# Performance work log

Hardware: AMD Instinct MI355X
Metric: run time of the kernel (lower is better)

The kernel has to match this reference:

```python
import jax, jax.numpy as jnp
import numpy as np

PATCH, STRIDE, TOPK, EPS = 16, 8, 8, 1e-8

def _leaky(x):
    return jax.nn.leaky_relu(x, 0.01)

def setup_inputs() -> dict:
    key = jax.random.key(0)
    ks = jax.random.split(key, 12)
    s = 0.05  # small weight scale to avoid tanh saturation
    return {
        "X":      jax.random.normal(ks[0], (16, 4096, 512), jnp.float32),
        "W_enc1": jax.random.normal(ks[1], (512, 256), jnp.float32) * s,
        "b_enc1": jax.random.normal(ks[2], (256,), jnp.float32) * s,
        "W_enc2": jax.random.normal(ks[3], (256, 64), jnp.float32) * s,
        "b_enc2": jax.random.normal(ks[4], (64,), jnp.float32) * s,
        "Wq":     jax.random.normal(ks[5], (64, 64), jnp.float32) * s,
        "Wk":     jax.random.normal(ks[6], (64, 64), jnp.float32) * s,
        "Wv":     jax.random.normal(ks[7], (64, 64), jnp.float32) * s,
        "W_agg":  jax.random.normal(ks[8], (64, 64), jnp.float32) * s,
        "b_agg":  jax.random.normal(ks[9], (64,), jnp.float32) * s,
        "W_dec":  jax.random.normal(ks[10], (64, 512), jnp.float32) * s,
        "b_dec":  jax.random.normal(ks[11], (512,), jnp.float32) * s,
    }

def reference(X, W_enc1, b_enc1, W_enc2, b_enc2, Wq, Wk, Wv, W_agg, b_agg, W_dec, b_dec):
    B, L, D = X.shape
    # var_encoder (dropout-free MLP)
    Xe = _leaky(X @ W_enc1 + b_enc1) @ W_enc2 + b_enc2          # (B, L, d)
    d = Xe.shape[-1]
    # unfold into overlapping patches
    h = (L - PATCH) // STRIDE + 1
    pos = jnp.arange(h)[:, None] * STRIDE + jnp.arange(PATCH)[None, :]  # (h, PATCH)
    patches = Xe[:, pos, :]                                      # (B, h, PATCH, d)
    per_patch = patches.mean(axis=2).reshape(B * h, d)           # (N, d)
    q = per_patch @ Wq
    k = per_patch @ Wk
    v = per_patch @ Wv                                           # (N, hqk)
    qn = q / (jnp.linalg.norm(q, axis=-1, keepdims=True) + EPS)
    kn = k / (jnp.linalg.norm(k, axis=-1, keepdims=True) + EPS)
    # antisymmetric outer product, (N, hqk, hqk)
    M = qn[:, :, None] * kn[:, None, :] - kn[:, :, None] * qn[:, None, :]
    A = jax.nn.relu(jnp.tanh(M))
    n = A.shape[-1]
    # topk pruning along last dim via scatter-style mask
    _, idx = jax.lax.top_k(A, TOPK)                              # (N, n, TOPK)
    mask = jnp.any(idx[..., None] == jnp.arange(n), axis=-2)     # (N, n, n) bool
    A = A * mask.astype(A.dtype)
    A = A / jnp.maximum(A.sum(axis=-1, keepdims=True), EPS)
    Av = jnp.einsum('nij,nj->ni', A, v)                          # (N, hqk)
    # after_agg (dropout = identity in eval)
    z = _leaky(Av @ W_agg + b_agg)                               # (N, d)
    zB = z.reshape(B, h, d)
    # overlap-add fold: each patch writes its (constant-over-time) z to its window
    seg = jnp.broadcast_to(zB[:, :, None, :], (B, h, PATCH, d)).reshape(B, h * PATCH, d)
    flat_pos = pos.reshape(-1)                                   # (h*PATCH,)
    out = jnp.zeros((B, L, d), X.dtype).at[:, flat_pos, :].add(seg)
    counts = jnp.zeros((L,), X.dtype).at[flat_pos].add(1.0)
    out = out / jnp.maximum(counts, 1.0)[None, :, None]
    return out @ W_dec + b_dec                                   # (B, L, D)
```

## Files before the change

### kernel.cpp

```cpp
#include <hip/hip_runtime.h>


typedef __attribute__((ext_vector_type(8))) _Float16 half8;
typedef __attribute__((ext_vector_type(4))) _Float16 half4;
typedef __attribute__((ext_vector_type(4))) float floatx4;

__device__ __forceinline__ _Float16 f2h(float f) { return (_Float16)f; }

#define MFMA16(A, B, C) __builtin_amdgcn_mfma_f32_16x16x32_f16((A), (B), (C), 0, 0, 0)

__global__ __launch_bounds__(256) void prep_weights(
    const float* __restrict__ W1, const float* __restrict__ W2,
    const float* __restrict__ Wd,
    _Float16* __restrict__ W1t, _Float16* __restrict__ W2t,
    _Float16* __restrict__ Wdt)
{
    int idx = blockIdx.x * 256 + threadIdx.x;
    { int n = idx >> 9, k = idx & 511;  W1t[idx] = f2h(W1[k * 256 + n]); }
    if (idx < 16384) { int n = idx >> 8, k = idx & 255; W2t[idx] = f2h(W2[k * 64 + n]); }
    if (idx < 32768) { int n = idx >> 6, k = idx & 63;  Wdt[idx] = f2h(Wd[k * 512 + n]); }
}

__global__ __launch_bounds__(256) void enc_fused(
    const float* __restrict__ X, const _Float16* __restrict__ W1t,
    const float* __restrict__ b1, const _Float16* __restrict__ W2t,
    const float* __restrict__ b2, float* __restrict__ Gs)
{
    __shared__ _Float16 smem[20992];
    _Float16* As   = smem;
    _Float16* Bs   = smem + 4608;
    _Float16* Hs16 = smem;

    const int tid  = threadIdx.x;
    const int lane = tid & 63;
    const int w    = tid >> 6;
    const int m0   = blockIdx.x * 64;

    const int arow  = tid >> 2;
    const int akseg = (tid & 3) << 4;
    const float* Abase = X + (size_t)(m0 + arow) * 512 + akseg;

    const int brow0  = (w << 6) + (lane >> 3);
    const int bchunk = (((lane & 7) ^ ((lane >> 3) & 7)) << 3);

    floatx4 acc1[4][4];
#pragma unroll
    for (int ci = 0; ci < 4; ci++)
#pragma unroll
        for (int mi = 0; mi < 4; mi++) acc1[ci][mi] = (floatx4){0.f, 0.f, 0.f, 0.f};

    float4 pa[4];
    auto loadA = [&](int kt) {
#pragma unroll
        for (int u = 0; u < 4; u++) pa[u] = *(const float4*)(Abase + kt + 4 * u);
    };

    loadA(0);
    for (int kt = 0; kt < 512; kt += 64) {
#pragma unroll
        for (int inst = 0; inst < 8; inst++) {
            const _Float16* src = W1t + (size_t)(brow0 + inst * 8) * 512 + kt + bchunk;
            __builtin_amdgcn_global_load_lds(
                (const __attribute__((address_space(1))) unsigned int*)src,
                (__attribute__((address_space(3))) unsigned int*)(Bs + ((w << 6) + inst * 8) * 64),
                16, 0, 0);
        }
        {
            _Float16* d = &As[arow * 72 + akseg];
#pragma unroll
            for (int h = 0; h < 2; h++) {
                float4 f0 = pa[2 * h], f1 = pa[2 * h + 1];
                half8 o;
                o[0] = f2h(f0.x); o[1] = f2h(f0.y); o[2] = f2h(f0.z); o[3] = f2h(f0.w);
                o[4] = f2h(f1.x); o[5] = f2h(f1.y); o[6] = f2h(f1.z); o[7] = f2h(f1.w);
                *(half8*)(d + 8 * h) = o;
            }
        }
        __syncthreads();
        if (kt + 64 < 512) loadA(kt + 64);
#pragma unroll
        for (int ks = 0; ks < 2; ks++) {
            const int lchunk = ks * 4 + (lane >> 4);
            half8 af[4], bf[4];
#pragma unroll
            for (int ci = 0; ci < 4; ci++) {
                const int c = (w << 6) + ci * 16 + (lane & 15);
                af[ci] = *(const half8*)&Bs[c * 64 + ((lchunk ^ (lane & 7)) << 3)];
            }
#pragma unroll
            for (int mi = 0; mi < 4; mi++)
                bf[mi] = *(const half8*)&As[(mi * 16 + (lane & 15)) * 72 + ks * 32 + ((lane >> 4) << 3)];
#pragma unroll
            for (int ci = 0; ci < 4; ci++)
#pragma unroll
                for (int mi = 0; mi < 4; mi++)
                    acc1[ci][mi] = MFMA16(af[ci], bf[mi], acc1[ci][mi]);
        }
        __syncthreads();
    }

    float4 b1v[4];
#pragma unroll
    for (int ci = 0; ci < 4; ci++)
        b1v[ci] = *(const float4*)&b1[(w << 6) + ci * 16 + ((lane >> 4) << 2)];
#pragma unroll
    for (int ci = 0; ci < 4; ci++) {
#pragma unroll
        for (int mi = 0; mi < 4; mi++) {
            float vs[4];
#pragma unroll
            for (int r = 0; r < 4; r++) {
                float v = acc1[ci][mi][r] + ((const float*)&b1v[ci])[r];
                vs[r] = v > 0.f ? v : 0.01f * v;
            }
#pragma unroll
            for (int r = 0; r < 4; r++) {
                vs[r] += __shfl_xor(vs[r], 1);
                vs[r] += __shfl_xor(vs[r], 2);
                vs[r] += __shfl_xor(vs[r], 4);
            }
            if ((lane & 7) == 0) {
                const int gl = 2 * mi + ((lane & 15) >> 3);
                half4 hv;
#pragma unroll
                for (int r = 0; r < 4; r++) hv[r] = f2h(vs[r]);
                *(half4*)&Hs16[gl * 264 + (w << 6) + ci * 16 + ((lane >> 4) << 2)] = hv;
            }
        }
    }
    __syncthreads();

    floatx4 acc2 = (floatx4){0.f, 0.f, 0.f, 0.f};
    const int kq = (lane >> 4) << 3;
#pragma unroll
    for (int ks = 0; ks < 8; ks++) {
        half8 af = *(const half8*)&Hs16[(lane & 15) * 264 + ks * 32 + kq];
        half8 bf = *(const half8*)&W2t[(size_t)((w << 4) + (lane & 15)) * 256 + ks * 32 + kq];
        acc2 = MFMA16(af, bf, acc2);
    }
    if (lane < 32) {
        const int n = (w << 4) + (lane & 15);
        const float bb = 8.f * b2[n];
        const int gbase = blockIdx.x * 8;
#pragma unroll
        for (int r = 0; r < 4; r++) {
            const int g = ((lane >> 4) << 2) + r;
            Gs[(size_t)(gbase + g) * 64 + n] = acc2[r] + bb;
        }
    }
}

#define TOP8_INS(mv) do { float _x = (mv); float _t;            \
    _t = fmaxf(s0,_x); _x = fminf(s0,_x); s0 = _t;              \
    _t = fmaxf(s1,_x); _x = fminf(s1,_x); s1 = _t;              \
    _t = fmaxf(s2,_x); _x = fminf(s2,_x); s2 = _t;              \
    _t = fmaxf(s3,_x); _x = fminf(s3,_x); s3 = _t;              \
    _t = fmaxf(s4,_x); _x = fminf(s4,_x); s4 = _t;              \
    _t = fmaxf(s5,_x); _x = fminf(s5,_x); s5 = _t;              \
    _t = fmaxf(s6,_x); _x = fminf(s6,_x); s6 = _t;              \
    s7 = fmaxf(s7,_x); } while (0)

__global__ __launch_bounds__(256) void patch_attn(
    const float* __restrict__ Gs,  const float* __restrict__ Wq,
    const float* __restrict__ Wk,  const float* __restrict__ Wv,
    const float* __restrict__ Wagg, const float* __restrict__ bagg,
    float* __restrict__ zout)
{
    __shared__ float sh[4][336];
    const int w    = threadIdx.x >> 6;
    const int lane = threadIdx.x & 63;
    const int n = blockIdx.x * 4 + w;
    const int b = n / 511;
    const int i = n - b * 511;
    float* pp  = &sh[w][0];
    float* qs  = pp + 64;
    float* ksm = pp + 128;
    float* vsm = pp + 192;
    float* avs = pp + 256;

    const float* gp = Gs + ((size_t)(b * 512 + i)) * 64 + lane;
    pp[lane] = (gp[0] + gp[64]) * 0.0625f;
    __syncthreads();

    float q = 0.f, k = 0.f, v = 0.f;
#pragma unroll 4
    for (int e = 0; e < 64; e += 4) {
        float4 p4 = *(const float4*)&pp[e];
        q = fmaf(p4.x, Wq[(e+0)*64+lane], q); q = fmaf(p4.y, Wq[(e+1)*64+lane], q);
        q = fmaf(p4.z, Wq[(e+2)*64+lane], q); q = fmaf(p4.w, Wq[(e+3)*64+lane], q);
        k = fmaf(p4.x, Wk[(e+0)*64+lane], k); k = fmaf(p4.y, Wk[(e+1)*64+lane], k);
        k = fmaf(p4.z, Wk[(e+2)*64+lane], k); k = fmaf(p4.w, Wk[(e+3)*64+lane], k);
        v = fmaf(p4.x, Wv[(e+0)*64+lane], v); v = fmaf(p4.y, Wv[(e+1)*64+lane], v);
        v = fmaf(p4.z, Wv[(e+2)*64+lane], v); v = fmaf(p4.w, Wv[(e+3)*64+lane], v);
    }
    float sq = q * q, sk = k * k;
#pragma unroll
    for (int o = 1; o < 64; o <<= 1) { sq += __shfl_xor(sq, o); sk += __shfl_xor(sk, o); }
    const float qni = q / (sqrtf(sq) + 1e-8f);
    const float kni = k / (sqrtf(sk) + 1e-8f);
    qs[lane] = qni; ksm[lane] = kni; vsm[lane] = v;
    __syncthreads();

    auto MV = [&](float kj, float qj) { return fmaf(qni, kj, -(kni * qj)); };

    float s0=-1e30f,s1=-1e30f,s2=-1e30f,s3=-1e30f,s4=-1e30f,s5=-1e30f,s6=-1e30f,s7=-1e30f;
#pragma unroll
    for (int j = 0; j < 64; j += 4) {
        float4 k4 = *(const float4*)&ksm[j];
        float4 q4 = *(const float4*)&qs[j];
        TOP8_INS(MV(k4.x, q4.x)); TOP8_INS(MV(k4.y, q4.y));
        TOP8_INS(MV(k4.z, q4.z)); TOP8_INS(MV(k4.w, q4.w));
    }
    const float teff = fmaxf(s7, 1e-37f) * (1.f - 1.2e-7f);

    float ssum = 0.f, av = 0.f;
#pragma unroll
    for (int j = 0; j < 64; j += 4) {
        float4 k4 = *(const float4*)&ksm[j];
        float4 q4 = *(const float4*)&qs[j];
        float4 v4 = *(const float4*)&vsm[j];
#define P2(KJ, QJ, VJ) do { float _m = MV(KJ, QJ); float _x2 = _m * _m;           \
        float _a = _m * (15.f + _x2) * __builtin_amdgcn_rcpf(fmaf(6.f, _x2, 15.f)); \
        float _am = (_m >= teff) ? _a : 0.f;                                       \
        ssum += _am; av = fmaf(_am, (VJ), av); } while (0)
        P2(k4.x, q4.x, v4.x); P2(k4.y, q4.y, v4.y);
        P2(k4.z, q4.z, v4.z); P2(k4.w, q4.w, v4.w);
#undef P2
    }
    avs[lane] = av / fmaxf(ssum, 1e-8f);
    __syncthreads();

    float zc = bagg[lane];
#pragma unroll 4
    for (int e = 0; e < 64; e += 4) {
        float4 a4 = *(const float4*)&avs[e];
        zc = fmaf(a4.x, Wagg[(e+0)*64+lane], zc); zc = fmaf(a4.y, Wagg[(e+1)*64+lane], zc);
        zc = fmaf(a4.z, Wagg[(e+2)*64+lane], zc); zc = fmaf(a4.w, Wagg[(e+3)*64+lane], zc);
    }
    zc = zc > 0.f ? zc : 0.01f * zc;
    zout[(size_t)n * 64 + lane] = zc;
}

__global__ __launch_bounds__(256) void dec_fused(
    const float* __restrict__ z, const _Float16* __restrict__ Wdt,
    const float* __restrict__ bd, float* __restrict__ out)
{
    __shared__ _Float16 As[128 * 72];
    __shared__ _Float16 Bs[128 * 72];
    const int tid  = threadIdx.x;
    const int lane = tid & 63;
    const int w    = tid >> 6;
    const int m0 = blockIdx.y * 128, n0 = blockIdx.x * 128;
    const int wrow = (w & 1) << 6, wcol = (w >> 1) << 6;

    {
        const int arow  = tid >> 1;
        const int akseg = (tid & 1) << 5;
        const int row = m0 + arow;
        const int b = row >> 12, l = row & 4095, g = l >> 3;
        const int g0 = g - 1 >= 0 ? g - 1 : 0;
        const int g1 = g <= 510 ? g : 510;
        const float w0 = (g >= 1) ? 1.f : 0.f;
        const float w1 = (g <= 510) ? 1.f : 0.f;
        const float sc = (w0 + w1) > 1.5f ? 0.5f : 1.f;
        const float* z0 = z + ((size_t)(b * 511 + g0)) * 64 + akseg;
        const float* z1 = z + ((size_t)(b * 511 + g1)) * 64 + akseg;
        _Float16* d = &As[arow * 72 + akseg];
#pragma unroll
        for (int u = 0; u < 4; u++) {
            float4 f0a = *(const float4*)(z0 + 8 * u);
            float4 f0b = *(const float4*)(z0 + 8 * u + 4);
            float4 f1a = *(const float4*)(z1 + 8 * u);
            float4 f1b = *(const float4*)(z1 + 8 * u + 4);
            half8 o;
            o[0] = f2h((f0a.x * w0 + f1a.x * w1) * sc);
            o[1] = f2h((f0a.y * w0 + f1a.y * w1) * sc);
            o[2] = f2h((f0a.z * w0 + f1a.z * w1) * sc);
            o[3] = f2h((f0a.w * w0 + f1a.w * w1) * sc);
            o[4] = f2h((f0b.x * w0 + f1b.x * w1) * sc);
            o[5] = f2h((f0b.y * w0 + f1b.y * w1) * sc);
            o[6] = f2h((f0b.z * w0 + f1b.z * w1) * sc);
            o[7] = f2h((f0b.w * w0 + f1b.w * w1) * sc);
            *(half8*)(d + 8 * u) = o;
        }
    }
    {
        const int brow  = tid >> 1;
        const int bkseg = (tid & 1) << 5;
        const _Float16* s = Wdt + (size_t)(n0 + brow) * 64 + bkseg;
        _Float16* d = &Bs[brow * 72 + bkseg];
#pragma unroll
        for (int u = 0; u < 4; u++) *(half8*)(d + 8 * u) = *(const half8*)(s + 8 * u);
    }
    __syncthreads();

    floatx4 accf[4][4];
#pragma unroll
    for (int mi = 0; mi < 4; mi++)
#pragma unroll
        for (int ni = 0; ni < 4; ni++) accf[mi][ni] = (floatx4){0.f, 0.f, 0.f, 0.f};
#pragma unroll
    for (int ks = 0; ks < 2; ks++) {
        const int koff = ks * 32 + ((lane >> 4) << 3);
        half8 af[4], bf[4];
#pragma unroll
        for (int mi = 0; mi < 4; mi++)
            af[mi] = *(const half8*)&As[(wrow + mi * 16 + (lane & 15)) * 72 + koff];
#pragma unroll
        for (int ni = 0; ni < 4; ni++)
            bf[ni] = *(const half8*)&Bs[(wcol + ni * 16 + (lane & 15)) * 72 + koff];
#pragma unroll
        for (int mi = 0; mi < 4; mi++)
#pragma unroll
            for (int ni = 0; ni < 4; ni++)
                accf[mi][ni] = MFMA16(af[mi], bf[ni], accf[mi][ni]);
    }

    float bvv[4];
#pragma unroll
    for (int ni = 0; ni < 4; ni++) bvv[ni] = bd[n0 + wcol + ni * 16 + (lane & 15)];

    float* Cs = (float*)As;
#pragma unroll
    for (int c = 0; c < 4; c++) {
        __syncthreads();
        const int own_wrow = ((c * 32) / 64) * 64;
        if (wrow == own_wrow) {
#pragma unroll
            for (int mm = 0; mm < 2; mm++) {
                const int mi = ((c * 32) % 64) / 16 + mm;
#pragma unroll
                for (int ni = 0; ni < 4; ni++) {
#pragma unroll
                    for (int r = 0; r < 4; r++) {
                        const int lr  = mm * 16 + ((lane >> 4) << 2) + r;
                        const int col = wcol + ni * 16 + (lane & 15);
                        Cs[lr * 128 + col] = accf[mi][ni][r] + bvv[ni];
                    }
                }
            }
        }
        __syncthreads();
#pragma unroll
        for (int u = 0; u < 4; u++) {
            const int idx = (u * 256 + tid) * 4;
            const int lr = idx >> 7, col = idx & 127;
            float4 vv = *(const float4*)&Cs[idx];
            *(float4*)&out[(size_t)(m0 + c * 32 + lr) * 512 + n0 + col] = vv;
        }
    }
}

extern "C" void kernel_launch(void* const* d_in, const int* in_sizes, int n_in,
                              void* d_out, int out_size, void* d_ws, size_t ws_size,
                              hipStream_t stream)
{
    const float* X    = (const float*)d_in[0];
    const float* W1   = (const float*)d_in[1];
    const float* b1   = (const float*)d_in[2];
    const float* W2   = (const float*)d_in[3];
    const float* b2   = (const float*)d_in[4];
    const float* Wq   = (const float*)d_in[5];
    const float* Wk   = (const float*)d_in[6];
    const float* Wv   = (const float*)d_in[7];
    const float* Wagg = (const float*)d_in[8];
    const float* bagg = (const float*)d_in[9];
    const float* Wd   = (const float*)d_in[10];
    const float* bd   = (const float*)d_in[11];

    char* ws = (char*)d_ws;
    float*    Gs  = (float*)(ws);
    float*    z   = (float*)(ws + 2097152);
    _Float16* W1t = (_Float16*)(ws + 4194304);
    _Float16* W2t = (_Float16*)(ws + 4456448);
    _Float16* Wdt = (_Float16*)(ws + 4489216);
    float* out = (float*)d_out;

    prep_weights<<<512, 256, 0, stream>>>(W1, W2, Wd, W1t, W2t, Wdt);
    enc_fused<<<1024, 256, 0, stream>>>(X, W1t, b1, W2t, b2, Gs);
    patch_attn<<<2044, 256, 0, stream>>>(Gs, Wq, Wk, Wv, Wagg, bagg, z);
    dec_fused<<<dim3(4, 512), 256, 0, stream>>>(z, Wdt, bd, out);
}
```

Baseline: 319.5 us.

## Double-buffer encoder GEMM LDS tiles and store decoder output directly

Restructures the first encoder GEMM k-loop from single-buffered 64-wide k tiles with two barriers per step into 32-wide double-buffered A/B LDS tiles with one barrier per step. The next W1 tile is fetched through global_load_lds and the next X tile is staged while MFMAs run on the current buffer, with a new XOR swizzle for the 32-wide B layout. Separately, the decoder epilogue drops the LDS-staged coalesced float4 store and writes accumulators straight to global memory. That removes barriers and LDS traffic but produces scalar, less coalesced 64-byte row segments for the large output.

```diff
diff --git a/kernel.cpp b/kernel.cpp
--- a/kernel.cpp
+++ b/kernel.cpp
@@ -26,9 +26,11 @@
     const float* __restrict__ b1, const _Float16* __restrict__ W2t,
     const float* __restrict__ b2, float* __restrict__ Gs)
 {
-    __shared__ _Float16 smem[20992];
-    _Float16* As   = smem;
-    _Float16* Bs   = smem + 4608;
+    __shared__ _Float16 smem[21504];
+    _Float16* As0  = smem;
+    _Float16* As1  = smem + 2560;
+    _Float16* Bs0  = smem + 5120;
+    _Float16* Bs1  = smem + 13312;
     _Float16* Hs16 = smem;
 
     const int tid  = threadIdx.x;
@@ -36,12 +38,9 @@
     const int w    = tid >> 6;
     const int m0   = blockIdx.x * 64;
 
-    const int arow  = tid >> 2;
-    const int akseg = (tid & 3) << 4;
-    const float* Abase = X + (size_t)(m0 + arow) * 512 + akseg;
-
-    const int brow0  = (w << 6) + (lane >> 3);
-    const int bchunk = (((lane & 7) ^ ((lane >> 3) & 7)) << 3);
+    const int arow = tid >> 2;
+    const int acol = (tid & 3) << 3;
+    const float* Abase = X + (size_t)(m0 + arow) * 512 + acol;
 
     floatx4 acc1[4][4];
 #pragma unroll
@@ -49,54 +48,65 @@
 #pragma unroll
         for (int mi = 0; mi < 4; mi++) acc1[ci][mi] = (floatx4){0.f, 0.f, 0.f, 0.f};
 
-    float4 pa[4];
+    float4 pa0, pa1;
     auto loadA = [&](int kt) {
-#pragma unroll
-        for (int u = 0; u < 4; u++) pa[u] = *(const float4*)(Abase + kt + 4 * u);
+        pa0 = *(const float4*)(Abase + kt);
+        pa1 = *(const float4*)(Abase + kt + 4);
     };
-
-    loadA(0);
-    for (int kt = 0; kt < 512; kt += 64) {
-#pragma unroll
-        for (int inst = 0; inst < 8; inst++) {
-            const _Float16* src = W1t + (size_t)(brow0 + inst * 8) * 512 + kt + bchunk;
+    auto writeAs = [&](_Float16* Ad) {
+        half8 o;
+        o[0] = f2h(pa0.x); o[1] = f2h(pa0.y); o[2] = f2h(pa0.z); o[3] = f2h(pa0.w);
+        o[4] = f2h(pa1.x); o[5] = f2h(pa1.y); o[6] = f2h(pa1.z); o[7] = f2h(pa1.w);
+        *(half8*)(Ad + arow * 40 + acol) = o;
+    };
+    auto issueB = [&](_Float16* Bd, int kt) {
+#pragma unroll
+        for (int q = 0; q < 4; q++) {
+            const int base_row = (w << 6) + (q << 4);
+            const int R  = base_row + (lane >> 2);
+            const int ch = lane & 3;
+            const _Float16* src = W1t + (size_t)R * 512 + kt + ((ch ^ ((R >> 1) & 3)) << 3);
             __builtin_amdgcn_global_load_lds(
                 (const __attribute__((address_space(1))) unsigned int*)src,
-                (__attribute__((address_space(3))) unsigned int*)(Bs + ((w << 6) + inst * 8) * 64),
+                (__attribute__((address_space(3))) unsigned int*)(Bd + base_row * 32),
                 16, 0, 0);
         }
-        {
-            _Float16* d = &As[arow * 72 + akseg];
-#pragma unroll
-            for (int h = 0; h < 2; h++) {
-                float4 f0 = pa[2 * h], f1 = pa[2 * h + 1];
-                half8 o;
-                o[0] = f2h(f0.x); o[1] = f2h(f0.y); o[2] = f2h(f0.z); o[3] = f2h(f0.w);
-                o[4] = f2h(f1.x); o[5] = f2h(f1.y); o[6] = f2h(f1.z); o[7] = f2h(f1.w);
-                *(half8*)(d + 8 * h) = o;
-            }
-        }
+    };
+
+    auto STEP = [&](_Float16* Ac, _Float16* Bc, _Float16* Aa, _Float16* Ba, int it) {
+        const int kt = it << 5;
+        if (it < 15) {
+            issueB(Ba, kt + 32);
+            writeAs(Aa);
+            if (it < 14) loadA(kt + 64);
+        }
+        const int kc  = lane >> 4;
+        half8 af[4], bf[4];
+#pragma unroll
+        for (int ci = 0; ci < 4; ci++) {
+            const int c = (w << 6) + ci * 16 + (lane & 15);
+            af[ci] = *(const half8*)&Bc[c * 32 + ((kc ^ ((c >> 1) & 3)) << 3)];
+        }
+#pragma unroll
+        for (int mi = 0; mi < 4; mi++)
+            bf[mi] = *(const half8*)&Ac[(mi * 16 + (lane & 15)) * 40 + (kc << 3)];
+#pragma unroll
+        for (int ci = 0; ci < 4; ci++)
+#pragma unroll
+            for (int mi = 0; mi < 4; mi++)
+                acc1[ci][mi] = MFMA16(af[ci], bf[mi], acc1[ci][mi]);
         __syncthreads();
-        if (kt + 64 < 512) loadA(kt + 64);
-#pragma unroll
-        for (int ks = 0; ks < 2; ks++) {
-            const int lchunk = ks * 4 + (lane >> 4);
-            half8 af[4], bf[4];
-#pragma unroll
-            for (int ci = 0; ci < 4; ci++) {
-                const int c = (w << 6) + ci * 16 + (lane & 15);
-                af[ci] = *(const half8*)&Bs[c * 64 + ((lchunk ^ (lane & 7)) << 3)];
-            }
-#pragma unroll
-            for (int mi = 0; mi < 4; mi++)
-                bf[mi] = *(const half8*)&As[(mi * 16 + (lane & 15)) * 72 + ks * 32 + ((lane >> 4) << 3)];
-#pragma unroll
-            for (int ci = 0; ci < 4; ci++)
-#pragma unroll
-                for (int mi = 0; mi < 4; mi++)
-                    acc1[ci][mi] = MFMA16(af[ci], bf[mi], acc1[ci][mi]);
-        }
-        __syncthreads();
+    };
+
+    loadA(0);
+    issueB(Bs0, 0);
+    writeAs(As0);
+    loadA(32);
+    __syncthreads();
+
+    for (int it = 0; it < 16; it += 2) {
+        STEP(As0, Bs0, As1, Bs1, it);
+        STEP(As1, Bs1, As0, Bs0, it + 1);
     }
 
     float4 b1v[4];
@@ -320,33 +330,15 @@
 #pragma unroll
     for (int ni = 0; ni < 4; ni++) bvv[ni] = bd[n0 + wcol + ni * 16 + (lane & 15)];
 
-    float* Cs = (float*)As;
-#pragma unroll
-    for (int c = 0; c < 4; c++) {
-        __syncthreads();
-        const int own_wrow = ((c * 32) / 64) * 64;
-        if (wrow == own_wrow) {
-#pragma unroll
-            for (int mm = 0; mm < 2; mm++) {
-                const int mi = ((c * 32) % 64) / 16 + mm;
-#pragma unroll
-                for (int ni = 0; ni < 4; ni++) {
-#pragma unroll
-                    for (int r = 0; r < 4; r++) {
-                        const int lr  = mm * 16 + ((lane >> 4) << 2) + r;
-                        const int col = wcol + ni * 16 + (lane & 15);
-                        Cs[lr * 128 + col] = accf[mi][ni][r] + bvv[ni];
-                    }
-                }
-            }
-        }
-        __syncthreads();
-#pragma unroll
-        for (int u = 0; u < 4; u++) {
-            const int idx = (u * 256 + tid) * 4;
-            const int lr = idx >> 7, col = idx & 127;
-            float4 vv = *(const float4*)&Cs[idx];
-            *(float4*)&out[(size_t)(m0 + c * 32 + lr) * 512 + n0 + col] = vv;
+#pragma unroll
+    for (int mi = 0; mi < 4; mi++) {
+        const int row = m0 + wrow + mi * 16 + ((lane >> 4) << 2);
+#pragma unroll
+        for (int r = 0; r < 4; r++) {
+            float* orow = out + (size_t)(row + r) * 512 + n0 + wcol + (lane & 15);
+#pragma unroll
+            for (int ni = 0; ni < 4; ni++)
+                orow[ni * 16] = accf[mi][ni][r] + bvv[ni];
         }
     }
 }
```

New measurement: 324.9 us. No clear change (+1.7%).
